# Optimization experiments

Measured on AMD Instinct MI355X. Metric: run time of the kernel, lower is better.

## Reference

```python
import jax, jax.numpy as jnp
import numpy as np

D = 1024      # atrybuty (d_model)
H = 16        # kanaly (heads)
DH = D // H   # head dim
B, T = 4, 2048
EPS = 1e-5


def setup_inputs() -> dict:
    key = jax.random.key(0)
    ks = jax.random.split(key, 16)
    s = 0.02
    return {
        "x":  jax.random.normal(ks[0], (B, T, D), jnp.float32),
        "wq": jax.random.normal(ks[1], (D, D), jnp.float32) * s,
        "wk": jax.random.normal(ks[2], (D, D), jnp.float32) * s,
        "wv": jax.random.normal(ks[3], (D, D), jnp.float32) * s,
        "wp": jax.random.normal(ks[4], (D, D), jnp.float32) * s,
        "bp": jnp.zeros((D,), jnp.float32),
        "w1": jax.random.normal(ks[5], (D, 4 * D), jnp.float32) * s,
        "b1": jnp.zeros((4 * D,), jnp.float32),
        "w2": jax.random.normal(ks[6], (4 * D, D), jnp.float32) * s,
        "b2": jnp.zeros((D,), jnp.float32),
        "g1": jnp.ones((D,), jnp.float32),
        "be1": jnp.zeros((D,), jnp.float32),
        "g2": jnp.ones((D,), jnp.float32),
        "be2": jnp.zeros((D,), jnp.float32),
    }


def _layernorm(x, g, b):
    mu = jnp.mean(x, axis=-1, keepdims=True)
    var = jnp.mean(jnp.square(x - mu), axis=-1, keepdims=True)
    return (x - mu) * jax.lax.rsqrt(var + EPS) * g + b


def reference(x, wq, wk, wv, wp, bp, w1, b1, w2, b2, g1, be1, g2, be2):
    b, t, d = x.shape
    # --- self-attention on ln1(x) ---
    h = _layernorm(x, g1, be1)
    # per-head Linears are equivalent to one [D,D] projection split into heads
    q = (h @ wq).reshape(b, t, H, DH).transpose(0, 2, 1, 3)  # [B,H,T,Dh]
    k = (h @ wk).reshape(b, t, H, DH).transpose(0, 2, 1, 3)
    v = (h @ wv).reshape(b, t, H, DH).transpose(0, 2, 1, 3)
    # NOTE: original scales by full embed dim C, not head_dim
    scale = jnp.asarray(d, x.dtype) ** -0.5
    wei = jnp.einsum("bhqd,bhkd->bhqk", q, k) * scale
    causal = jnp.tril(jnp.ones((t, t), bool))
    wei = jnp.where(causal, wei, -jnp.inf)
    wei = jax.nn.softmax(wei, axis=-1)
    att = jnp.einsum("bhqk,bhkd->bhqd", wei, v)
    att = att.transpose(0, 2, 1, 3).reshape(b, t, d)
    x = x + att @ wp + bp
    # --- feedforward on ln2(x) ---
    h2 = _layernorm(x, g2, be2)
    x = x + jax.nn.relu(h2 @ w1 + b1) @ w2 + b2
    return x
```

## Files before the change

kernel.cpp:

```cpp
#include <hip/hip_runtime.h>
#include <hip/hip_bf16.h>
#include <stdint.h>

#define DM   1024
#define NH   16
#define DH   64
#define BATCH 4
#define SEQ  2048
#define MROWS (BATCH*SEQ)

typedef float f32x4 __attribute__((ext_vector_type(4)));
typedef __bf16 bf16x8 __attribute__((ext_vector_type(8)));
typedef short s16x4 __attribute__((ext_vector_type(4)));
typedef int   i32x2 __attribute__((ext_vector_type(2)));

#define QSCALE 0.045084220f

#define VM(n) asm volatile("s_waitcnt vmcnt(" #n ")" ::: "memory")
#define LGKM0 do { asm volatile("s_waitcnt lgkmcnt(0)" ::: "memory"); \
                   __builtin_amdgcn_sched_barrier(0); } while (0)

__device__ __forceinline__ short f2bs(float f) {
    __bf16 h = (__bf16)f;
    return __builtin_bit_cast(short, h);
}

__device__ __forceinline__ void gload_lds16(const void* g, void* l) {
    __builtin_amdgcn_global_load_lds(
        (__attribute__((address_space(1))) void*)(g),
        (__attribute__((address_space(3))) void*)(l), 16, 0, 0);
}

__device__ __forceinline__ void swz_xy(int ny, int& x, int& y) {
    const int bid = blockIdx.x;
    const int cpx = gridDim.x >> 3;
    const int wg  = (bid & 7) * cpx + (bid >> 3);
    x = wg / ny;
    y = wg % ny;
}

__global__ __launch_bounds__(256) void transpose_cvt_kernel(
    const float* __restrict__ w, short* __restrict__ wt, int K, int N)
{
    __shared__ short tile[64 * 65];
    const int k0 = blockIdx.x * 64, n0 = blockIdx.y * 64;
    const int t = threadIdx.x;
#pragma unroll
    for (int i = 0; i < 16; ++i) {
        int idx = i * 256 + t;
        int r = idx >> 6, c = idx & 63;
        tile[r * 65 + c] = f2bs(w[(size_t)(k0 + r) * N + n0 + c]);
    }
    __syncthreads();
#pragma unroll
    for (int i = 0; i < 16; ++i) {
        int idx = i * 256 + t;
        int r = idx >> 6, c = idx & 63;
        wt[(size_t)(n0 + r) * K + k0 + c] = tile[c * 65 + r];
    }
}

__global__ __launch_bounds__(256) void ln_kernel(
    const float* __restrict__ x, const float* __restrict__ g,
    const float* __restrict__ be, short* __restrict__ out)
{
    const int row = blockIdx.x, t = threadIdx.x;
    const float4 v = ((const float4*)(x + (size_t)row * DM))[t];
    float s  = v.x + v.y + v.z + v.w;
    float ss = v.x * v.x + v.y * v.y + v.z * v.z + v.w * v.w;
#pragma unroll
    for (int d = 1; d < 64; d <<= 1) {
        s  += __shfl_xor(s, d, 64);
        ss += __shfl_xor(ss, d, 64);
    }
    __shared__ float red[8];
    const int wid = t >> 6;
    if ((t & 63) == 0) { red[wid] = s; red[wid + 4] = ss; }
    __syncthreads();
    s  = red[0] + red[1] + red[2] + red[3];
    ss = red[4] + red[5] + red[6] + red[7];
    const float mu = s * (1.0f / DM);
    const float rs = rsqrtf(ss * (1.0f / DM) - mu * mu + 1e-5f);
    const float4 gg = ((const float4*)g)[t];
    const float4 bb = ((const float4*)be)[t];
    short4 o;
    o.x = f2bs((v.x - mu) * rs * gg.x + bb.x);
    o.y = f2bs((v.y - mu) * rs * gg.y + bb.y);
    o.z = f2bs((v.z - mu) * rs * gg.z + bb.z);
    o.w = f2bs((v.w - mu) * rs * gg.w + bb.w);
    ((short4*)(out + (size_t)row * DM))[t] = o;
}

template<int NCHUNK>
__device__ __forceinline__ void stage32(
    const short* __restrict__ G, int ldk, int row0, int k0,
    short* __restrict__ lds, int t)
{
#pragma unroll
    for (int i = 0; i < NCHUNK / 512; ++i) {
        const int c  = i * 512 + t;
        const int r  = c >> 2;
        const int sl = (c & 3) ^ ((r >> 1) & 3);
        gload_lds16(&G[(size_t)(row0 + r) * ldk + k0 + sl * 8], &lds[c * 8]);
    }
}

template<int EPI>
__global__ __launch_bounds__(512) void gemm256(
    const short* __restrict__ A, const short* __restrict__ Bt,
    int N, int K, int nyT,
    const float* __restrict__ bias, short* __restrict__ outb,
    short* __restrict__ qo, short* __restrict__ ko, short* __restrict__ vo)
{
    __shared__ short As[4][8192];
    __shared__ short Bs[4][8192];
    const int t = threadIdx.x, lane = t & 63, w = t >> 6;
    const int l15 = lane & 15, hi = lane >> 4;
    const int wm = (w >> 2) * 128, wn = (w & 3) * 64;
    int bx, by; swz_xy(nyT, bx, by);
    const int m0 = bx * 256, n0 = by * 256;
    const int NT = K >> 5;

    f32x4 acc[8][4] = {};

    stage32<1024>(A, K, m0, 0,  As[0], t); stage32<1024>(Bt, K, n0, 0,  Bs[0], t);
    stage32<1024>(A, K, m0, 32, As[1], t); stage32<1024>(Bt, K, n0, 32, Bs[1], t);
    stage32<1024>(A, K, m0, 64, As[2], t); stage32<1024>(Bt, K, n0, 64, Bs[2], t);
    VM(8);
    __builtin_amdgcn_s_barrier();

    for (int kt = 0; kt < NT; ++kt) {
        const short* Ac = As[kt & 3];
        const short* Bc = Bs[kt & 3];
        const int k3 = (kt + 3) << 5;
        bf16x8 af[8], bfr[4];

#pragma unroll
        for (int fm = 0; fm < 4; ++fm) {
            const int r = wm + fm * 16 + l15;
            af[fm] = *(const bf16x8*)&Ac[r * 32 + ((hi ^ ((r >> 1) & 3)) << 3)];
        }
#pragma unroll
        for (int fn = 0; fn < 4; ++fn) {
            const int r = wn + fn * 16 + l15;
            bfr[fn] = *(const bf16x8*)&Bc[r * 32 + ((hi ^ ((r >> 1) & 3)) << 3)];
        }
        if (kt + 3 < NT) stage32<1024>(A, K, m0, k3, As[(kt + 3) & 3], t);
        __builtin_amdgcn_s_barrier();
        LGKM0;
        __builtin_amdgcn_s_setprio(1);
#pragma unroll
        for (int fm = 0; fm < 4; ++fm)
#pragma unroll
            for (int fn = 0; fn < 4; ++fn)
                acc[fm][fn] = __builtin_amdgcn_mfma_f32_16x16x32_bf16(
                    af[fm], bfr[fn], acc[fm][fn], 0, 0, 0);
        __builtin_amdgcn_s_setprio(0);
        __builtin_amdgcn_s_barrier();

#pragma unroll
        for (int fm = 4; fm < 8; ++fm) {
            const int r = wm + fm * 16 + l15;
            af[fm] = *(const bf16x8*)&Ac[r * 32 + ((hi ^ ((r >> 1) & 3)) << 3)];
        }
        if (kt + 3 < NT) {
            stage32<1024>(Bt, K, n0, k3, Bs[(kt + 3) & 3], t);
            VM(8);
        } else if (kt + 2 < NT) VM(4);
        else if (kt + 1 < NT) VM(0);
        __builtin_amdgcn_s_barrier();
        LGKM0;
        __builtin_amdgcn_s_setprio(1);
#pragma unroll
        for (int fm = 4; fm < 8; ++fm)
#pragma unroll
            for (int fn = 0; fn < 4; ++fn)
                acc[fm][fn] = __builtin_amdgcn_mfma_f32_16x16x32_bf16(
                    af[fm], bfr[fn], acc[fm][fn], 0, 0, 0);
        __builtin_amdgcn_s_setprio(0);
        __builtin_amdgcn_s_barrier();
    }

#pragma unroll
    for (int fm = 0; fm < 8; ++fm)
#pragma unroll
        for (int fn = 0; fn < 4; ++fn) {
            const int row0 = m0 + wm + fm * 16 + hi * 4;
            const int nn = n0 + wn + fn * 16 + l15;
            const f32x4 a = acc[fm][fn];
            if constexpr (EPI == 0) {
                const int mat = nn >> 10, n1 = nn & 1023;
                const int head = n1 >> 6, dh = n1 & 63;
                if (mat == 2) {
                    const int tok = row0 & 2047, b = row0 >> 11;
                    const int tokp = (tok & ~63) |
                        (((((tok >> 3) & 7) ^ (dh & 7)) << 3)) | (tok & 7);
                    short4 pk;
                    pk.x = f2bs(a[0]); pk.y = f2bs(a[1]);
                    pk.z = f2bs(a[2]); pk.w = f2bs(a[3]);
                    *(short4*)&vo[((size_t)(b * NH + head) * DH + dh) * SEQ + tokp] = pk;
                } else if (mat == 1) {
#pragma unroll
                    for (int rr = 0; rr < 4; ++rr) {
                        const int m = row0 + rr;
                        const int b = m >> 11, tok = m & 2047;
                        const int dhp = (((dh >> 3) ^ (tok & 7)) << 3) | (dh & 7);
                        ko[((size_t)(b * NH + head) * SEQ + tok) * DH + dhp] =
                            f2bs(a[rr]);
                    }
                } else {
#pragma unroll
                    for (int rr = 0; rr < 4; ++rr) {
                        const int m = row0 + rr;
                        const int b = m >> 11, tok = m & 2047;
                        qo[((size_t)(b * NH + head) * SEQ + tok) * DH + dh] =
                            f2bs(a[rr] * QSCALE);
                    }
                }
            } else {
                const float bb = bias[nn];
#pragma unroll
                for (int rr = 0; rr < 4; ++rr) {
                    const float z = a[rr] + bb;
                    outb[(size_t)(row0 + rr) * N + nn] = f2bs(z > 0.f ? z : 0.f);
                }
            }
        }
}

__global__ __launch_bounds__(256) void gemm_bt128(
    const short* __restrict__ A, const short* __restrict__ Bt,
    int N, int K, int nyT,
    const float* __restrict__ bias, const float* __restrict__ res,
    float* __restrict__ outf)
{
    __shared__ short As[4][4096];
    __shared__ short Bs[4][4096];
    const int t = threadIdx.x, lane = t & 63, w = t >> 6;
    const int l15 = lane & 15, hi = lane >> 4;
    const int wm = (w & 1) * 64, wn = (w >> 1) * 64;
    int bx, by; swz_xy(nyT, bx, by);
    const int m0 = bx * 128, n0 = by * 128;
    const int NT = K >> 5;

    f32x4 acc[4][4] = {};

#define STAGE128(G, row0, k0, lds)                                            \
    do {                                                                      \
        _Pragma("unroll")                                                     \
        for (int i2 = 0; i2 < 2; ++i2) {                                      \
            const int c  = i2 * 256 + t;                                      \
            const int r  = c >> 2;                                            \
            const int sl = (c & 3) ^ ((r >> 1) & 3);                          \
            gload_lds16(&(G)[(size_t)((row0) + r) * K + (k0) + sl * 8],       \
                        &(lds)[c * 8]);                                       \
        }                                                                     \
    } while (0)

    STAGE128(A, m0, 0,  As[0]); STAGE128(Bt, n0, 0,  Bs[0]);
    STAGE128(A, m0, 32, As[1]); STAGE128(Bt, n0, 32, Bs[1]);
    STAGE128(A, m0, 64, As[2]); STAGE128(Bt, n0, 64, Bs[2]);

    for (int kt = 0; kt < NT; ++kt) {
        if (kt + 2 < NT) VM(8);
        else if (kt + 1 < NT) VM(4);
        else VM(0);
        __builtin_amdgcn_s_barrier();

        const short* Ac = As[kt & 3];
        const short* Bc = Bs[kt & 3];
        bf16x8 af[4], bfr[4];
#pragma unroll
        for (int fm = 0; fm < 4; ++fm) {
            const int r = wm + fm * 16 + l15;
            af[fm] = *(const bf16x8*)&Ac[r * 32 + ((hi ^ ((r >> 1) & 3)) << 3)];
        }
#pragma unroll
        for (int fn = 0; fn < 4; ++fn) {
            const int r = wn + fn * 16 + l15;
            bfr[fn] = *(const bf16x8*)&Bc[r * 32 + ((hi ^ ((r >> 1) & 3)) << 3)];
        }
#pragma unroll
        for (int fm = 0; fm < 4; ++fm)
#pragma unroll
            for (int fn = 0; fn < 4; ++fn)
                acc[fm][fn] = __builtin_amdgcn_mfma_f32_16x16x32_bf16(
                    af[fm], bfr[fn], acc[fm][fn], 0, 0, 0);

        __builtin_amdgcn_s_barrier();
        if (kt + 3 < NT) {
            STAGE128(A,  m0, (kt + 3) << 5, As[(kt + 3) & 3]);
            STAGE128(Bt, n0, (kt + 3) << 5, Bs[(kt + 3) & 3]);
        }
    }
#undef STAGE128

#pragma unroll
    for (int fm = 0; fm < 4; ++fm)
#pragma unroll
        for (int fn = 0; fn < 4; ++fn) {
            const int row0 = m0 + wm + fm * 16 + hi * 4;
            const int nn = n0 + wn + fn * 16 + l15;
            const float bb = bias[nn];
            const f32x4 a = acc[fm][fn];
#pragma unroll
            for (int rr = 0; rr < 4; ++rr) {
                const int m = row0 + rr;
                outf[(size_t)m * N + nn] = a[rr] + bb + res[(size_t)m * N + nn];
            }
        }
}

__global__ __launch_bounds__(512) void attn_kernel(
    const short* __restrict__ Q, const short* __restrict__ Kx,
    const short* __restrict__ Vt, short* __restrict__ att)
{
    __shared__ short Ks[2][2][4096];
    __shared__ short Vs[2][2][4096];

    const int n  = blockIdx.x;
    const int bh = n & 63;
    const int j  = n >> 6;
    const int qb = (j < 4) ? (7 - j) : (j - 4);
    const int tid = threadIdx.x;
    const int lane = tid & 63;
    const int wq = tid >> 6;
    const int l15 = lane & 15, hi = lane >> 4;
    const int qw = qb * 256 + wq * 32;
    const size_t base  = (size_t)bh * (SEQ * DH);
    const size_t vbase = (size_t)bh * (DH * SEQ);
    const int b = bh >> 4, head = bh & 15;

    bf16x8 qf[2][2];
#pragma unroll
    for (int mf = 0; mf < 2; ++mf)
#pragma unroll
        for (int kf = 0; kf < 2; ++kf)
            qf[mf][kf] = *(const bf16x8*)
                &Q[base + (size_t)(qw + mf * 16 + l15) * DH + kf * 32 + hi * 8];

    f32x4 O[2][4] = {};
    float L[2] = {0.f, 0.f};

    const int nkv_blk = 4 * qb + 4;
    const int ndt     = nkv_blk >> 1;
    const int nkv_wv  = (qw + 95) >> 6;

#define STAGE_KV2(DT, BUF)                                                     \
    do {                                                                       \
        const int kvo = (DT) * 128;                                            \
        const int rw = tid >> 3, sl = tid & 7;                                 \
        _Pragma("unroll")                                                      \
        for (int sb = 0; sb < 2; ++sb) {                                       \
            gload_lds16(&Kx[base + (size_t)(kvo + sb * 64 + rw) * DH + sl * 8],\
                        &Ks[BUF][sb][tid * 8]);                                \
            gload_lds16(&Vt[vbase + (size_t)rw * SEQ + kvo + sb * 64 + sl * 8],\
                        &Vs[BUF][sb][tid * 8]);                                \
        }                                                                      \
    } while (0)

    STAGE_KV2(0, 0);

    for (int dt = 0; dt < ndt; ++dt) {
        VM(0);
        __builtin_amdgcn_s_barrier();
        if (dt + 1 < ndt) STAGE_KV2(dt + 1, (dt + 1) & 1);

#pragma unroll
        for (int sb = 0; sb < 2; ++sb) {
            const int t2 = dt * 2 + sb;
            if (t2 >= nkv_wv) break;
            const short* Kc = &Ks[dt & 1][sb][0];
            const short* Vc = &Vs[dt & 1][sb][0];
            const int kv0 = t2 * 64;

            bf16x8 kfr[4][2];
#pragma unroll
            for (int nf = 0; nf < 4; ++nf)
#pragma unroll
                for (int kf = 0; kf < 2; ++kf)
                    kfr[nf][kf] = *(const bf16x8*)
                        &Kc[(nf * 16 + l15) * 64 + (((kf * 4 + hi) ^ (l15 & 7)) << 3)];

            f32x4 St[4][2] = {};
#pragma unroll
            for (int kf = 0; kf < 2; ++kf)
#pragma unroll
                for (int nf = 0; nf < 4; ++nf)
#pragma unroll
                    for (int mf = 0; mf < 2; ++mf)
                        St[nf][mf] = __builtin_amdgcn_mfma_f32_16x16x32_bf16(
                            kfr[nf][kf], qf[mf][kf], St[nf][mf], 0, 0, 0);

            if (kv0 + 63 > qw) {
#pragma unroll
                for (int mf = 0; mf < 2; ++mf) {
                    const int q = qw + mf * 16 + l15;
#pragma unroll
                    for (int nf = 0; nf < 4; ++nf)
#pragma unroll
                        for (int r = 0; r < 4; ++r) {
                            const int kv = kv0 + nf * 16 + hi * 4 + r;
                            if (kv > q) St[nf][mf][r] = -3.0e38f;
                        }
                }
            }

            float lp[2] = {0.f, 0.f};
            s16x4 pa[4][2];
#pragma unroll
            for (int nf = 0; nf < 4; ++nf)
#pragma unroll
                for (int mf = 0; mf < 2; ++mf) {
                    const float p0 = exp2f(St[nf][mf][0]);
                    const float p1 = exp2f(St[nf][mf][1]);
                    const float p2 = exp2f(St[nf][mf][2]);
                    const float p3 = exp2f(St[nf][mf][3]);
                    lp[mf] += (p0 + p1) + (p2 + p3);
                    unsigned dw0, dw1;
                    asm("v_cvt_pk_bf16_f32 %0, %1, %2" : "=v"(dw0) : "v"(p0), "v"(p1));
                    asm("v_cvt_pk_bf16_f32 %0, %1, %2" : "=v"(dw1) : "v"(p2), "v"(p3));
                    i32x2 dd; dd[0] = (int)dw0; dd[1] = (int)dw1;
                    pa[nf][mf] = __builtin_bit_cast(s16x4, dd);
                }
            L[0] += lp[0]; L[1] += lp[1];

#pragma unroll
            for (int nf = 0; nf < 4; ++nf)
#pragma unroll
                for (int jf = 0; jf < 4; ++jf) {
                    const s16x4 vfr = *(const s16x4*)
                        &Vc[(jf * 16 + l15) * 64 +
                            ((((nf * 2 + (hi >> 1)) ^ (l15 & 7)) << 3) + ((hi & 1) << 2))];
#pragma unroll
                    for (int mf = 0; mf < 2; ++mf)
                        O[mf][jf] = __builtin_amdgcn_mfma_f32_16x16x16bf16_1k(
                            pa[nf][mf], vfr, O[mf][jf], 0, 0, 0);
                }
        }
    }
#undef STAGE_KV2

#pragma unroll
    for (int mf = 0; mf < 2; ++mf) {
        L[mf] += __shfl_xor(L[mf], 16, 64);
        L[mf] += __shfl_xor(L[mf], 32, 64);
    }
    const float inv0 = 1.0f / L[0], inv1 = 1.0f / L[1];

#pragma unroll
    for (int mf = 0; mf < 2; ++mf) {
        const float invm = mf ? inv1 : inv0;
#pragma unroll
        for (int r = 0; r < 4; ++r) {
            const int addr = ((lane >> 4) << 4) + (r << 2);
            const float iv = __builtin_bit_cast(float,
                __builtin_amdgcn_ds_bpermute(addr, __builtin_bit_cast(int, invm)));
            const int q = qw + mf * 16 + hi * 4 + r;
#pragma unroll
            for (int jf = 0; jf < 4; ++jf)
                att[(size_t)(b * SEQ + q) * DM + head * DH + jf * 16 + l15] =
                    f2bs(O[mf][jf][r] * iv);
        }
    }
}

extern "C" void kernel_launch(void* const* d_in, const int* in_sizes, int n_in,
                              void* d_out, int out_size, void* d_ws, size_t ws_size,
                              hipStream_t stream) {
    const float* x   = (const float*)d_in[0];
    const float* wq  = (const float*)d_in[1];
    const float* wk  = (const float*)d_in[2];
    const float* wv  = (const float*)d_in[3];
    const float* wp  = (const float*)d_in[4];
    const float* bp  = (const float*)d_in[5];
    const float* w1  = (const float*)d_in[6];
    const float* b1  = (const float*)d_in[7];
    const float* w2  = (const float*)d_in[8];
    const float* b2  = (const float*)d_in[9];
    const float* g1  = (const float*)d_in[10];
    const float* be1 = (const float*)d_in[11];
    const float* g2  = (const float*)d_in[12];
    const float* be2 = (const float*)d_in[13];
    float* out = (float*)d_out;

    char* ws = (char*)d_ws;
    short* wqkv_t = (short*)(ws + 0);
    short* wp_t   = (short*)(ws + 6291456);
    short* w1_t   = (short*)(ws + 8388608);
    short* w2_t   = (short*)(ws + 16777216);
    short* h      = (short*)(ws + 25165824);
    short* qb     = (short*)(ws + 41943040);
    short* kb     = (short*)(ws + 58720256);
    short* vb     = (short*)(ws + 75497472);
    short* att    = (short*)(ws + 92274688);
    float* x1     = (float*)(ws + 109051904);
    short* h2     = (short*)(ws + 142606336);
    short* tbuf   = (short*)(ws + 25165824);

    dim3 blk(256);

    transpose_cvt_kernel<<<dim3(16, 16), blk, 0, stream>>>(wq, wqkv_t,                1024, 1024);
    transpose_cvt_kernel<<<dim3(16, 16), blk, 0, stream>>>(wk, wqkv_t + 1024 * 1024,  1024, 1024);
    transpose_cvt_kernel<<<dim3(16, 16), blk, 0, stream>>>(wv, wqkv_t + 2048 * 1024,  1024, 1024);
    transpose_cvt_kernel<<<dim3(16, 16), blk, 0, stream>>>(wp, wp_t,                  1024, 1024);
    transpose_cvt_kernel<<<dim3(16, 64), blk, 0, stream>>>(w1, w1_t,                  1024, 4096);
    transpose_cvt_kernel<<<dim3(64, 16), blk, 0, stream>>>(w2, w2_t,                  4096, 1024);

    ln_kernel<<<MROWS, blk, 0, stream>>>(x, g1, be1, h);

    gemm256<0><<<dim3(384), dim3(512), 0, stream>>>(h, wqkv_t, 3072, 1024, 12,
        nullptr, nullptr, qb, kb, vb);

    attn_kernel<<<dim3(512), dim3(512), 0, stream>>>(qb, kb, vb, att);

    gemm_bt128<<<dim3(512), blk, 0, stream>>>(att, wp_t, 1024, 1024, 8,
        bp, x, x1);

    ln_kernel<<<MROWS, blk, 0, stream>>>(x1, g2, be2, h2);

    gemm256<2><<<dim3(512), dim3(512), 0, stream>>>(h2, w1_t, 4096, 1024, 16,
        b1, tbuf, nullptr, nullptr, nullptr);

    gemm_bt128<<<dim3(512), blk, 0, stream>>>(tbuf, w2_t, 1024, 4096, 8,
        b2, x1, out);
}
```

Measured before the change: 383.0 us.

## Replace 128x128 output GEMM with 256x64 tiles using two waves

The N=1024 output GEMMs (attention projection and FFN down-projection) change from 128x128 tiles with four waves to 256x64 tiles with two waves. Each wave now computes 128x64 with 32 accumulators, and the pipeline goes from four LDS buffers to three. The goal is fewer B-operand loads per FLOP and a different wave/tile balance, at the cost of fewer waves per block, higher register use and less latency hiding. The grid stays at 512 blocks.

```diff
diff --git a/kernel.cpp b/kernel.cpp
--- a/kernel.cpp
+++ b/kernel.cpp
@@ -228,79 +228,82 @@
         }
 }
 
-__global__ __launch_bounds__(256) void gemm_bt128(
+__global__ __launch_bounds__(128) void gemm_wide(
     const short* __restrict__ A, const short* __restrict__ Bt,
     int N, int K, int nyT,
     const float* __restrict__ bias, const float* __restrict__ res,
     float* __restrict__ outf)
 {
-    __shared__ short As[4][4096];
-    __shared__ short Bs[4][4096];
+    __shared__ short As[3][8192];
+    __shared__ short Bs[3][2048];
     const int t = threadIdx.x, lane = t & 63, w = t >> 6;
     const int l15 = lane & 15, hi = lane >> 4;
-    const int wm = (w & 1) * 64, wn = (w >> 1) * 64;
+    const int wm = w * 128;
     int bx, by; swz_xy(nyT, bx, by);
-    const int m0 = bx * 128, n0 = by * 128;
+    const int m0 = bx * 256, n0 = by * 64;
     const int NT = K >> 5;
 
-    f32x4 acc[4][4] = {};
-
-#define STAGE128(G, row0, k0, lds)                                            \
+    f32x4 acc[8][4] = {};
+
+#define STAGEW(k0, buf)                                                       \
     do {                                                                      \
         _Pragma("unroll")                                                     \
-        for (int i2 = 0; i2 < 2; ++i2) {                                      \
-            const int c  = i2 * 256 + t;                                      \
+        for (int i2 = 0; i2 < 8; ++i2) {                                      \
+            const int c  = i2 * 128 + t;                                      \
             const int r  = c >> 2;                                            \
             const int sl = (c & 3) ^ ((r >> 1) & 3);                          \
-            gload_lds16(&(G)[(size_t)((row0) + r) * K + (k0) + sl * 8],       \
-                        &(lds)[c * 8]);                                       \
+            gload_lds16(&A[(size_t)(m0 + r) * K + (k0) + sl * 8],             \
+                        &As[buf][c * 8]);                                     \
+        }                                                                     \
+        _Pragma("unroll")                                                     \
+        for (int i2 = 0; i2 < 2; ++i2) {                                      \
+            const int c  = i2 * 128 + t;                                      \
+            const int r  = c >> 2;                                            \
+            const int sl = (c & 3) ^ ((r >> 1) & 3);                          \
+            gload_lds16(&Bt[(size_t)(n0 + r) * K + (k0) + sl * 8],            \
+                        &Bs[buf][c * 8]);                                     \
         }                                                                     \
     } while (0)
 
-    STAGE128(A, m0, 0,  As[0]); STAGE128(Bt, n0, 0,  Bs[0]);
-    STAGE128(A, m0, 32, As[1]); STAGE128(Bt, n0, 32, Bs[1]);
-    STAGE128(A, m0, 64, As[2]); STAGE128(Bt, n0, 64, Bs[2]);
+    STAGEW(0, 0); STAGEW(32, 1); STAGEW(64, 2);
 
     for (int kt = 0; kt < NT; ++kt) {
-        if (kt + 2 < NT) VM(8);
-        else if (kt + 1 < NT) VM(4);
+        if (kt + 2 < NT) VM(20);
+        else if (kt + 1 < NT) VM(10);
         else VM(0);
         __builtin_amdgcn_s_barrier();
 
-        const short* Ac = As[kt & 3];
-        const short* Bc = Bs[kt & 3];
-        bf16x8 af[4], bfr[4];
-#pragma unroll
-        for (int fm = 0; fm < 4; ++fm) {
+        const short* Ac = As[kt % 3];
+        const short* Bc = Bs[kt % 3];
+        bf16x8 af[8], bfr[4];
+#pragma unroll
+        for (int fm = 0; fm < 8; ++fm) {
             const int r = wm + fm * 16 + l15;
             af[fm] = *(const bf16x8*)&Ac[r * 32 + ((hi ^ ((r >> 1) & 3)) << 3)];
         }
 #pragma unroll
         for (int fn = 0; fn < 4; ++fn) {
-            const int r = wn + fn * 16 + l15;
+            const int r = fn * 16 + l15;
             bfr[fn] = *(const bf16x8*)&Bc[r * 32 + ((hi ^ ((r >> 1) & 3)) << 3)];
         }
 #pragma unroll
-        for (int fm = 0; fm < 4; ++fm)
+        for (int fm = 0; fm < 8; ++fm)
 #pragma unroll
             for (int fn = 0; fn < 4; ++fn)
                 acc[fm][fn] = __builtin_amdgcn_mfma_f32_16x16x32_bf16(
                     af[fm], bfr[fn], acc[fm][fn], 0, 0, 0);
 
         __builtin_amdgcn_s_barrier();
-        if (kt + 3 < NT) {
-            STAGE128(A,  m0, (kt + 3) << 5, As[(kt + 3) & 3]);
-            STAGE128(Bt, n0, (kt + 3) << 5, Bs[(kt + 3) & 3]);
-        }
-    }
-#undef STAGE128
-
-#pragma unroll
-    for (int fm = 0; fm < 4; ++fm)
+        if (kt + 3 < NT) STAGEW((kt + 3) << 5, kt % 3);
+    }
+#undef STAGEW
+
+#pragma unroll
+    for (int fm = 0; fm < 8; ++fm)
 #pragma unroll
         for (int fn = 0; fn < 4; ++fn) {
             const int row0 = m0 + wm + fm * 16 + hi * 4;
-            const int nn = n0 + wn + fn * 16 + l15;
+            const int nn = n0 + fn * 16 + l15;
             const float bb = bias[nn];
             const f32x4 a = acc[fm][fn];
 #pragma unroll
@@ -514,7 +517,7 @@
 
     attn_kernel<<<dim3(512), dim3(512), 0, stream>>>(qb, kb, vb, att);
 
-    gemm_bt128<<<dim3(512), blk, 0, stream>>>(att, wp_t, 1024, 1024, 8,
+    gemm_wide<<<dim3(512), dim3(128), 0, stream>>>(att, wp_t, 1024, 1024, 16,
         bp, x, x1);
 
     ln_kernel<<<MROWS, blk, 0, stream>>>(x1, g2, be2, h2);
@@ -522,6 +525,6 @@
     gemm256<2><<<dim3(512), dim3(512), 0, stream>>>(h2, w1_t, 4096, 1024, 16,
         b1, tbuf, nullptr, nullptr, nullptr);
 
-    gemm_bt128<<<dim3(512), blk, 0, stream>>>(tbuf, w2_t, 1024, 4096, 8,
+    gemm_wide<<<dim3(512), dim3(128), 0, stream>>>(tbuf, w2_t, 1024, 4096, 16,
         b2, x1, out);
 }
```

After: 430.8 us. 12.5% more time.

## Use BK=64 double-buffered LDS pipeline in residual-output GEMM

Applied to the files above, without the earlier changes.

Replaces the 4-stage BK=32 prefetch pipeline in gemm_bt128 with a 2-stage BK=64 double buffer. Each iteration first issues the next tile's global-to-LDS loads, then computes the current tile. The LDS swizzle changes to an 8-way XOR suited to 64-wide rows. Doubling K per iteration halves the number of barriers and loop iterations, at the cost of shallower prefetch depth and less latency hiding.

```diff
diff --git a/kernel.cpp b/kernel.cpp
--- a/kernel.cpp
+++ b/kernel.cpp
@@ -234,66 +234,73 @@
     const float* __restrict__ bias, const float* __restrict__ res,
     float* __restrict__ outf)
 {
-    __shared__ short As[4][4096];
-    __shared__ short Bs[4][4096];
+    __shared__ short As[2][8192];
+    __shared__ short Bs[2][8192];
     const int t = threadIdx.x, lane = t & 63, w = t >> 6;
     const int l15 = lane & 15, hi = lane >> 4;
     const int wm = (w & 1) * 64, wn = (w >> 1) * 64;
     int bx, by; swz_xy(nyT, bx, by);
     const int m0 = bx * 128, n0 = by * 128;
-    const int NT = K >> 5;
+    const int NT = K >> 6;
 
     f32x4 acc[4][4] = {};
 
-#define STAGE128(G, row0, k0, lds)                                            \
+#define STAGE64(G, row0, k0, lds)                                             \
     do {                                                                      \
         _Pragma("unroll")                                                     \
-        for (int i2 = 0; i2 < 2; ++i2) {                                      \
+        for (int i2 = 0; i2 < 4; ++i2) {                                      \
             const int c  = i2 * 256 + t;                                      \
-            const int r  = c >> 2;                                            \
-            const int sl = (c & 3) ^ ((r >> 1) & 3);                          \
+            const int r  = c >> 3;                                            \
+            const int sl = (c & 7) ^ (r & 7);                                 \
             gload_lds16(&(G)[(size_t)((row0) + r) * K + (k0) + sl * 8],       \
                         &(lds)[c * 8]);                                       \
         }                                                                     \
     } while (0)
 
-    STAGE128(A, m0, 0,  As[0]); STAGE128(Bt, n0, 0,  Bs[0]);
-    STAGE128(A, m0, 32, As[1]); STAGE128(Bt, n0, 32, Bs[1]);
-    STAGE128(A, m0, 64, As[2]); STAGE128(Bt, n0, 64, Bs[2]);
+    STAGE64(A, m0, 0, As[0]);
+    STAGE64(Bt, n0, 0, Bs[0]);
 
     for (int kt = 0; kt < NT; ++kt) {
-        if (kt + 2 < NT) VM(8);
-        else if (kt + 1 < NT) VM(4);
-        else VM(0);
-        __builtin_amdgcn_s_barrier();
-
-        const short* Ac = As[kt & 3];
-        const short* Bc = Bs[kt & 3];
-        bf16x8 af[4], bfr[4];
+        if (kt + 1 < NT) {
+            STAGE64(A,  m0, (kt + 1) << 6, As[(kt + 1) & 1]);
+            STAGE64(Bt, n0, (kt + 1) << 6, Bs[(kt + 1) & 1]);
+            VM(8);
+        } else {
+            VM(0);
+        }
+        __builtin_amdgcn_s_barrier();
+
+        const short* Ac = As[kt & 1];
+        const short* Bc = Bs[kt & 1];
+        bf16x8 af[4][2], bfr[4][2];
 #pragma unroll
         for (int fm = 0; fm < 4; ++fm) {
             const int r = wm + fm * 16 + l15;
-            af[fm] = *(const bf16x8*)&Ac[r * 32 + ((hi ^ ((r >> 1) & 3)) << 3)];
+#pragma unroll
+            for (int ks = 0; ks < 2; ++ks)
+                af[fm][ks] = *(const bf16x8*)
+                    &Ac[r * 64 + (((ks * 4 + hi) ^ (r & 7)) << 3)];
         }
 #pragma unroll
         for (int fn = 0; fn < 4; ++fn) {
             const int r = wn + fn * 16 + l15;
-            bfr[fn] = *(const bf16x8*)&Bc[r * 32 + ((hi ^ ((r >> 1) & 3)) << 3)];
-        }
-#pragma unroll
-        for (int fm = 0; fm < 4; ++fm)
-#pragma unroll
-            for (int fn = 0; fn < 4; ++fn)
-                acc[fm][fn] = __builtin_amdgcn_mfma_f32_16x16x32_bf16(
-                    af[fm], bfr[fn], acc[fm][fn], 0, 0, 0);
-
-        __builtin_amdgcn_s_barrier();
-        if (kt + 3 < NT) {
-            STAGE128(A,  m0, (kt + 3) << 5, As[(kt + 3) & 3]);
-            STAGE128(Bt, n0, (kt + 3) << 5, Bs[(kt + 3) & 3]);
-        }
-    }
-#undef STAGE128
+#pragma unroll
+            for (int ks = 0; ks < 2; ++ks)
+                bfr[fn][ks] = *(const bf16x8*)
+                    &Bc[r * 64 + (((ks * 4 + hi) ^ (r & 7)) << 3)];
+        }
+#pragma unroll
+        for (int ks = 0; ks < 2; ++ks)
+#pragma unroll
+            for (int fm = 0; fm < 4; ++fm)
+#pragma unroll
+                for (int fn = 0; fn < 4; ++fn)
+                    acc[fm][fn] = __builtin_amdgcn_mfma_f32_16x16x32_bf16(
+                        af[fm][ks], bfr[fn][ks], acc[fm][fn], 0, 0, 0);
+
+        __builtin_amdgcn_s_barrier();
+    }
+#undef STAGE64
 
 #pragma unroll
     for (int fm = 0; fm < 4; ++fm)
```

New measurement: 367.6 us. 4.0% less time.
